# Kernel tuning notes

Measured on AMD Instinct MI355X. Metric: run time of the kernel, lower is better.

## Reference

```python
import jax, jax.numpy as jnp
import numpy as np

SHAPES = [(96, 96), (48, 48), (24, 24), (12, 12)]
B, C, NH, NP, NL, LYR, DFF = 4, 256, 8, 3, 4, 3, 1024
HD = C // NH
N = sum(h * w for h, w in SHAPES)


def setup_inputs():
    ks = iter(jax.random.split(jax.random.key(0), 64))
    p = lambda shape, s=0.02: jax.random.normal(next(ks), shape, jnp.float32) * s
    d = {}
    for i, (h, w) in enumerate(SHAPES):
        d[f'src{i}'] = jax.random.normal(next(ks), (B, C, h, w), jnp.float32)
        d[f'mask{i}'] = jnp.zeros((B, h, w), jnp.bool_)
        d[f'pos{i}'] = jax.random.normal(next(ks), (B, C, h, w), jnp.float32) * 0.02
    d['level_embed'] = p((NL, C), 1.0)  # torch init: normal_(std=1)
    d['W_off'] = p((LYR, C, NH * NL * NP * 2), 0.05); d['b_off'] = p((LYR, NH * NL * NP * 2), 0.05)
    d['W_attw'] = p((LYR, C, NH * NL * NP)); d['b_attw'] = jnp.zeros((LYR, NH * NL * NP))
    d['W_val'] = p((LYR, C, C)); d['b_val'] = jnp.zeros((LYR, C))
    d['W_out'] = p((LYR, C, C)); d['b_out'] = jnp.zeros((LYR, C))
    d['ln1_g'] = jnp.ones((LYR, C)); d['ln1_b'] = jnp.zeros((LYR, C))
    d['W_ff1'] = p((LYR, C, DFF)); d['b_ff1'] = jnp.zeros((LYR, DFF))
    d['W_ff2'] = p((LYR, DFF, C)); d['b_ff2'] = jnp.zeros((LYR, C))
    d['ln2_g'] = jnp.ones((LYR, C)); d['ln2_b'] = jnp.zeros((LYR, C))
    d['lnf_g'] = jnp.ones((C,)); d['lnf_b'] = jnp.zeros((C,))
    return d


def _layer_norm(x, g, b, eps=1e-5):
    m = jnp.mean(x, -1, keepdims=True)
    v = jnp.var(x, -1, keepdims=True)
    return (x - m) * jax.lax.rsqrt(v + eps) * g + b


def _ref_points():
    # centers of each cell per level, normalized to [0,1]; xy order -> [N,4] boxes with wh=0.1
    pts = []
    for h, w in SHAPES:
        ys = (jnp.arange(h, dtype=jnp.float32) + 0.5) / h
        xs = (jnp.arange(w, dtype=jnp.float32) + 0.5) / w
        yy, xx = jnp.meshgrid(ys, xs, indexing='ij')
        pts.append(jnp.stack([xx.ravel(), yy.ravel()], -1))
    r = jnp.concatenate(pts, 0)
    return jnp.concatenate([r, jnp.full_like(r, 0.1)], -1)


def _bilinear(value, H, W, loc):
    # value [B,H*W,NH,HD]; loc [B,Q,NH,NP,2] normalized; align_corners=False, zero padding
    x = loc[..., 0] * W - 0.5
    y = loc[..., 1] * H - 0.5
    x0f = jnp.floor(x); y0f = jnp.floor(y)
    wx = x - x0f; wy = y - y0f
    x0 = x0f.astype(jnp.int32); y0 = y0f.astype(jnp.int32)
    vt = jnp.transpose(value, (0, 2, 1, 3))  # [B,NH,HW,HD]
    Bq, Q = loc.shape[0], loc.shape[1]

    def g(yi, xi):
        valid = ((xi >= 0) & (xi < W) & (yi >= 0) & (yi < H)).astype(value.dtype)
        idx = jnp.clip(yi, 0, H - 1) * W + jnp.clip(xi, 0, W - 1)  # [B,Q,NH,NP]
        it = jnp.transpose(idx, (0, 2, 1, 3)).reshape(Bq, NH, Q * NP, 1)
        it = jnp.broadcast_to(it, (Bq, NH, Q * NP, HD))
        v = jnp.take_along_axis(vt, it, axis=2).reshape(Bq, NH, Q, NP, HD)
        v = jnp.transpose(v, (0, 2, 1, 3, 4))  # [B,Q,NH,NP,HD]
        return v * valid[..., None]

    return (g(y0, x0) * ((1 - wy) * (1 - wx))[..., None]
            + g(y0, x0 + 1) * ((1 - wy) * wx)[..., None]
            + g(y0 + 1, x0) * (wy * (1 - wx))[..., None]
            + g(y0 + 1, x0 + 1) * (wy * wx)[..., None])


def _msda(q, x, mask, ref, l, W_off, b_off, W_attw, b_attw, W_val, b_val, W_out, b_out):
    Bq, Nq, _ = q.shape
    value = x @ W_val[l] + b_val[l]
    value = jnp.where(mask[..., None], 0.0, value).reshape(Bq, Nq, NH, HD)
    off = (q @ W_off[l] + b_off[l]).reshape(Bq, Nq, NH, NL, NP, 2)
    aw = jax.nn.softmax((q @ W_attw[l] + b_attw[l]).reshape(Bq, Nq, NH, NL * NP), -1)
    aw = aw.reshape(Bq, Nq, NH, NL, NP)
    ref_xy = ref[None, :, None, None, None, :2]
    ref_wh = ref[None, :, None, None, None, 2:]
    loc = ref_xy + off / NP * ref_wh * 0.5  # [B,N,NH,NL,NP,2]
    out = jnp.zeros((Bq, Nq, NH, HD), x.dtype)
    s0 = 0
    for li, (h, w) in enumerate(SHAPES):
        samp = _bilinear(value[:, s0:s0 + h * w], h, w, loc[:, :, :, li])
        out = out + jnp.einsum('bqhpd,bqhp->bqhd', samp, aw[:, :, :, li])
        s0 += h * w
    return out.reshape(Bq, Nq, C) @ W_out[l] + b_out[l]


def _forward(srcs, masks, poss, level_embed, W_off, b_off, W_attw, b_attw, W_val, b_val,
             W_out, b_out, ln1_g, ln1_b, W_ff1, b_ff1, W_ff2, b_ff2, ln2_g, ln2_b, lnf_g, lnf_b):
    x = jnp.concatenate([s.reshape(B, C, -1).transpose(0, 2, 1) for s in srcs], 1)  # [B,N,C]
    mf = jnp.concatenate([m.reshape(B, -1) for m in masks], 1)                      # [B,N]
    pf = jnp.concatenate([p_.reshape(B, C, -1).transpose(0, 2, 1) + level_embed[i]
                          for i, p_ in enumerate(poss)], 1)
    ref = _ref_points()
    for l in range(LYR):
        q = x + pf
        x2 = _msda(q, x, mf, ref, l, W_off, b_off, W_attw, b_attw, W_val, b_val, W_out, b_out)
        x = _layer_norm(x + x2, ln1_g[l], ln1_b[l])
        h = jax.nn.gelu(x @ W_ff1[l] + b_ff1[l], approximate=False)
        x = _layer_norm(x + h @ W_ff2[l] + b_ff2[l], ln2_g[l], ln2_b[l])
    return _layer_norm(x, lnf_g, lnf_b)


def reference(src0, src1, src2, src3, mask0, mask1, mask2, mask3, pos0, pos1, pos2, pos3,
              level_embed, W_off, b_off, W_attw, b_attw, W_val, b_val, W_out, b_out,
              ln1_g, ln1_b, W_ff1, b_ff1, W_ff2, b_ff2, ln2_g, ln2_b, lnf_g, lnf_b):
    return _forward([src0, src1, src2, src3], [mask0, mask1, mask2, mask3],
                    [pos0, pos1, pos2, pos3], level_embed, W_off, b_off, W_attw, b_attw,
                    W_val, b_val, W_out, b_out, ln1_g, ln1_b, W_ff1, b_ff1, W_ff2, b_ff2,
                    ln2_g, ln2_b, lnf_g, lnf_b)
```

## Files before the change

### kernel.cpp

```cpp
#include <hip/hip_runtime.h>

#define B_   4
#define C_   256
#define NH_  8
#define HD_  32
#define NP_  3
#define NL_  4
#define LYR_ 3
#define DFF_ 1024
#define N_   12240
#define M_   (B_*N_)
#define MP_  49152
#define LT_  729088

typedef __attribute__((ext_vector_type(8))) short short8;
typedef __attribute__((ext_vector_type(4))) float f32x4;

__device__ __forceinline__ unsigned short f2bf(float f) {
    union { float f; unsigned u; } v; v.f = f;
    unsigned r = (v.u + 0x7fffu + ((v.u >> 16) & 1u)) >> 16;
    return (unsigned short)r;
}
__device__ __forceinline__ float bf2f(unsigned short h) {
    union { unsigned u; float f; } v; v.u = ((unsigned)h) << 16;
    return v.f;
}

__global__ __launch_bounds__(256) void k_concat(
    const float* __restrict__ s0, const float* __restrict__ s1,
    const float* __restrict__ s2, const float* __restrict__ s3,
    const float* __restrict__ p0, const float* __restrict__ p1,
    const float* __restrict__ p2, const float* __restrict__ p3,
    const float* __restrict__ lev, float* __restrict__ x, float* __restrict__ pf)
{
    int idx = blockIdx.x * 256 + threadIdx.x;
    int c  = idx & (C_ - 1);
    int bn = idx >> 8;
    int n  = bn % N_;
    int b  = bn / N_;
    int li, s, HW; const float *sp, *pp;
    if (n < 9216)       { li = 0; s = n;         HW = 9216; sp = s0; pp = p0; }
    else if (n < 11520) { li = 1; s = n - 9216;  HW = 2304; sp = s1; pp = p1; }
    else if (n < 12096) { li = 2; s = n - 11520; HW = 576;  sp = s2; pp = p2; }
    else                { li = 3; s = n - 12096; HW = 144;  sp = s3; pp = p3; }
    size_t o = (size_t)(b * C_ + c) * HW + s;
    x[idx]  = sp[o];
    pf[idx] = pp[o] + lev[li * C_ + c];
}

__global__ __launch_bounds__(256) void k_mask(
    float* __restrict__ v,
    const unsigned char* __restrict__ m0, const unsigned char* __restrict__ m1,
    const unsigned char* __restrict__ m2, const unsigned char* __restrict__ m3)
{
    int row = blockIdx.x;
    int n = row % N_, b = row / N_;
    int s, HW; const unsigned char* mp;
    if (n < 9216)       { s = n;         HW = 9216; mp = m0; }
    else if (n < 11520) { s = n - 9216;  HW = 2304; mp = m1; }
    else if (n < 12096) { s = n - 11520; HW = 576;  mp = m2; }
    else                { s = n - 12096; HW = 144;  mp = m3; }
    if (mp[b * HW + s])
        v[(size_t)row * C_ + threadIdx.x] = 0.f;
}

__global__ __launch_bounds__(256) void k_split(
    const float* __restrict__ W, unsigned short* __restrict__ Th,
    unsigned short* __restrict__ Tl, int K, int N)
{
    int per = K * N;
    int idx = blockIdx.x * 256 + threadIdx.x;
    if (idx >= LYR_ * per) return;
    int l = idx / per, r = idx - l * per;
    int k = r / N, n = r - k * N;
    float v = W[idx];
    unsigned short h = f2bf(v);
    unsigned short lo = f2bf(v - bf2f(h));
    size_t o = (size_t)l * LT_ + (size_t)n * K + k;
    Th[o] = h; Tl[o] = lo;
}

__device__ __forceinline__ int swz(int row, int bcol) {
    return row * 128 + (bcol ^ ((row & 7) << 4));
}

template <int MODE, bool ADD2>
__global__ __launch_bounds__(256) void k_mgemm(
    const float* __restrict__ A, const float* __restrict__ A2,
    const unsigned short* __restrict__ Bh, const unsigned short* __restrict__ Bl,
    const float* __restrict__ bias, const float* __restrict__ bias2, int bsplit,
    float* __restrict__ Cm, int Ndim, int Kdim)
{
    __shared__ __align__(16) unsigned short Ahs[128 * 64];
    __shared__ __align__(16) unsigned short Als[128 * 64];
    __shared__ __align__(16) unsigned short Bhs[128 * 64];
    __shared__ __align__(16) unsigned short Bls[128 * 64];

    const int tid = threadIdx.x;
    const int bm = blockIdx.y * 128;
    const int bn = blockIdx.x * 128;
    const int w  = tid >> 6, lane = tid & 63;
    const int wr = w >> 1, wc = w & 1;
    const int lm = lane & 15, lg = lane >> 4;

    const int srow = tid >> 1;
    const int sbc  = (tid & 1) * 64;

    f32x4 acc[4][4] = {};

    for (int k0 = 0; k0 < Kdim; k0 += 64) {
        {
            const float* Ap  = A  + (size_t)(bm + srow) * Kdim + k0 + (sbc >> 1);
            const float* A2p = A2 + (size_t)(bm + srow) * Kdim + k0 + (sbc >> 1);
            #pragma unroll
            for (int q = 0; q < 4; ++q) {
                float4 v0 = *(const float4*)(Ap + q * 8);
                float4 v1 = *(const float4*)(Ap + q * 8 + 4);
                if (ADD2) {
                    float4 u0 = *(const float4*)(A2p + q * 8);
                    float4 u1 = *(const float4*)(A2p + q * 8 + 4);
                    v0.x += u0.x; v0.y += u0.y; v0.z += u0.z; v0.w += u0.w;
                    v1.x += u1.x; v1.y += u1.y; v1.z += u1.z; v1.w += u1.w;
                }
                float f[8] = {v0.x, v0.y, v0.z, v0.w, v1.x, v1.y, v1.z, v1.w};
                short8 hv, lv;
                #pragma unroll
                for (int j = 0; j < 8; ++j) {
                    unsigned short h = f2bf(f[j]);
                    hv[j] = (short)h;
                    lv[j] = (short)f2bf(f[j] - bf2f(h));
                }
                int o = swz(srow, sbc + q * 16) >> 1;
                *(short8*)&Ahs[o] = hv;
                *(short8*)&Als[o] = lv;
            }
        }
        {
            int ng = bn + srow;
            bool ok = ng < Ndim;
            const unsigned short* bhp = Bh + (size_t)ng * Kdim + k0 + (sbc >> 1);
            const unsigned short* blp = Bl + (size_t)ng * Kdim + k0 + (sbc >> 1);
            #pragma unroll
            for (int q = 0; q < 4; ++q) {
                short8 hv = {}, lv = {};
                if (ok) {
                    hv = *(const short8*)(bhp + q * 8);
                    lv = *(const short8*)(blp + q * 8);
                }
                int o = swz(srow, sbc + q * 16) >> 1;
                *(short8*)&Bhs[o] = hv;
                *(short8*)&Bls[o] = lv;
            }
        }
        __syncthreads();
        #pragma unroll
        for (int ks = 0; ks < 2; ++ks) {
            const int cb = ks * 64 + lg * 16;
            short8 ah[4], al[4], bh[4], bl[4];
            #pragma unroll
            for (int i = 0; i < 4; ++i) {
                int o = swz(wr * 64 + i * 16 + lm, cb) >> 1;
                ah[i] = *(const short8*)&Ahs[o];
                al[i] = *(const short8*)&Als[o];
            }
            #pragma unroll
            for (int j = 0; j < 4; ++j) {
                int o = swz(wc * 64 + j * 16 + lm, cb) >> 1;
                bh[j] = *(const short8*)&Bhs[o];
                bl[j] = *(const short8*)&Bls[o];
            }
            #pragma unroll
            for (int i = 0; i < 4; ++i)
                #pragma unroll
                for (int j = 0; j < 4; ++j) {
                    acc[i][j] = __builtin_amdgcn_mfma_f32_16x16x32_bf16(al[i], bh[j], acc[i][j], 0, 0, 0);
                    acc[i][j] = __builtin_amdgcn_mfma_f32_16x16x32_bf16(ah[i], bl[j], acc[i][j], 0, 0, 0);
                    acc[i][j] = __builtin_amdgcn_mfma_f32_16x16x32_bf16(ah[i], bh[j], acc[i][j], 0, 0, 0);
                }
        }
        __syncthreads();
    }

    #pragma unroll
    for (int j = 0; j < 4; ++j) {
        int col = bn + wc * 64 + j * 16 + lm;
        if (col < Ndim) {
            float bb = (col < bsplit) ? bias[col] : bias2[col - bsplit];
            #pragma unroll
            for (int i = 0; i < 4; ++i) {
                #pragma unroll
                for (int p = 0; p < 4; ++p) {
                    int row = bm + wr * 64 + i * 16 + lg * 4 + p;
                    float v = acc[i][j][p] + bb;
                    if (MODE == 1)
                        v = 0.5f * v * (1.f + erff(v * 0.70710678118654752f));
                    Cm[(size_t)row * Ndim + col] = v;
                }
            }
        }
    }
}

__global__ __launch_bounds__(256) void k_sample(
    const float* __restrict__ value, const float* __restrict__ comb,
    float* __restrict__ out)
{
    int t = blockIdx.x * 256 + threadIdx.x;
    int gid = t >> 3, q4 = t & 3 * 2 + (t & 7);
    gid = t >> 3; q4 = t & 7;
    int h  = gid & 7;
    int bn = gid >> 3;
    int n  = bn % N_;
    int b  = bn / N_;

    int sr, Wr;
    if (n < 9216)       { sr = n;         Wr = 96; }
    else if (n < 11520) { sr = n - 9216;  Wr = 48; }
    else if (n < 12096) { sr = n - 11520; Wr = 24; }
    else                { sr = n - 12096; Wr = 12; }
    int iy = sr / Wr, ix = sr % Wr;
    float refx = (ix + 0.5f) / Wr;
    float refy = (iy + 0.5f) / Wr;

    const float* rowp = comb + (size_t)bn * 288;
    const float* offp = rowp + h * 24;
    const float* lgp  = rowp + 192 + h * 12;

    float lv[12];
    float mx = lgp[0];
    lv[0] = mx;
    #pragma unroll
    for (int i = 1; i < 12; ++i) { lv[i] = lgp[i]; mx = fmaxf(mx, lv[i]); }
    float ssum = 0.f;
    #pragma unroll
    for (int i = 0; i < 12; ++i) { lv[i] = __expf(lv[i] - mx); ssum += lv[i]; }
    float sinv = 1.f / ssum;

    const float* vbase = value + ((size_t)b * N_) * C_ + h * HD_ + q4 * 4;

    float4 acc = make_float4(0.f, 0.f, 0.f, 0.f);
    int s0 = 0;
    #pragma unroll
    for (int li = 0; li < 4; ++li) {
        const int Wl = 96 >> li;
        #pragma unroll
        for (int p = 0; p < NP_; ++p) {
            float ox = offp[(li * NP_ + p) * 2 + 0];
            float oy = offp[(li * NP_ + p) * 2 + 1];
            float xf = (refx + ox * (1.f / 60.f)) * Wl - 0.5f;
            float yf = (refy + oy * (1.f / 60.f)) * Wl - 0.5f;
            float x0f = floorf(xf), y0f = floorf(yf);
            float wx = xf - x0f, wy = yf - y0f;
            int x0 = (int)x0f, y0 = (int)y0f;
            float a = lv[li * NP_ + p] * sinv;
            #pragma unroll
            for (int dy = 0; dy < 2; ++dy) {
                #pragma unroll
                for (int dx = 0; dx < 2; ++dx) {
                    int yi = y0 + dy, xi = x0 + dx;
                    if (xi >= 0 && xi < Wl && yi >= 0 && yi < Wl) {
                        float wgt = a * (dy ? wy : 1.f - wy) * (dx ? wx : 1.f - wx);
                        float4 v = *(const float4*)(vbase + (size_t)(s0 + yi * Wl + xi) * C_);
                        acc.x += wgt * v.x; acc.y += wgt * v.y;
                        acc.z += wgt * v.z; acc.w += wgt * v.w;
                    }
                }
            }
        }
        s0 += Wl * Wl;
    }
    *(float4*)(out + (size_t)gid * HD_ + q4 * 4) = acc;
}

__global__ __launch_bounds__(256) void k_add_ln(
    const float* __restrict__ xin, const float* __restrict__ r,
    const float* __restrict__ g, const float* __restrict__ bta,
    float* __restrict__ out)
{
    int row = blockIdx.x;
    int c = threadIdx.x;
    size_t o = (size_t)row * C_ + c;
    float v = xin[o] + (r ? r[o] : 0.f);
    float s1 = v, s2 = v * v;
    #pragma unroll
    for (int ofs = 32; ofs > 0; ofs >>= 1) {
        s1 += __shfl_down(s1, ofs);
        s2 += __shfl_down(s2, ofs);
    }
    __shared__ float r1[4], r2[4];
    int wid = threadIdx.x >> 6, lane = threadIdx.x & 63;
    if (lane == 0) { r1[wid] = s1; r2[wid] = s2; }
    __syncthreads();
    float m   = (r1[0] + r1[1] + r1[2] + r1[3]) * (1.f / C_);
    float var = (r2[0] + r2[1] + r2[2] + r2[3]) * (1.f / C_) - m * m;
    float inv = rsqrtf(var + 1e-5f);
    out[o] = (v - m) * inv * g[c] + bta[c];
}

extern "C" void kernel_launch(void* const* d_in, const int* in_sizes, int n_in,
                              void* d_out, int out_size, void* d_ws, size_t ws_size,
                              hipStream_t stream)
{
    const float* src0 = (const float*)d_in[0];
    const unsigned char* mask0 = (const unsigned char*)d_in[1];
    const float* pos0 = (const float*)d_in[2];
    const float* src1 = (const float*)d_in[3];
    const unsigned char* mask1 = (const unsigned char*)d_in[4];
    const float* pos1 = (const float*)d_in[5];
    const float* src2 = (const float*)d_in[6];
    const unsigned char* mask2 = (const unsigned char*)d_in[7];
    const float* pos2 = (const float*)d_in[8];
    const float* src3 = (const float*)d_in[9];
    const unsigned char* mask3 = (const unsigned char*)d_in[10];
    const float* pos3 = (const float*)d_in[11];
    const float* lev    = (const float*)d_in[12];
    const float* W_off  = (const float*)d_in[13];
    const float* b_off  = (const float*)d_in[14];
    const float* W_attw = (const float*)d_in[15];
    const float* b_attw = (const float*)d_in[16];
    const float* W_val  = (const float*)d_in[17];
    const float* b_val  = (const float*)d_in[18];
    const float* W_out  = (const float*)d_in[19];
    const float* b_out  = (const float*)d_in[20];
    const float* ln1_g  = (const float*)d_in[21];
    const float* ln1_b  = (const float*)d_in[22];
    const float* W_ff1  = (const float*)d_in[23];
    const float* b_ff1  = (const float*)d_in[24];
    const float* W_ff2  = (const float*)d_in[25];
    const float* b_ff2  = (const float*)d_in[26];
    const float* ln2_g  = (const float*)d_in[27];
    const float* ln2_b  = (const float*)d_in[28];
    const float* lnf_g  = (const float*)d_in[29];
    const float* lnf_b  = (const float*)d_in[30];

    float* ws = (float*)d_ws;
    auto at = [&](size_t u) { return ws + u * (size_t)MP_; };
    float* x    = at(0);
    float* pf   = at(256);
    float* val  = at(512);
    float* msda = at(768);
    float* comb = at(1024);
    float* tmp  = at(1024);
    float* hbuf = at(512);

    unsigned short* Wh = (unsigned short*)(ws + (size_t)1312 * MP_);
    unsigned short* Wl = Wh + (size_t)LYR_ * LT_;
    const size_t OF_VAL = 0, OF_CMB = 65536, OF_ATT = 114688,
                 OF_OUT = 139264, OF_F1 = 204800, OF_F2 = 466944;

    const dim3 T(256);
    const int BIG = 1 << 30;

    k_split<<<(LYR_*65536 + 255)/256, T, 0, stream>>>(W_val,  Wh + OF_VAL, Wl + OF_VAL, 256, 256);
    k_split<<<(LYR_*49152 + 255)/256, T, 0, stream>>>(W_off,  Wh + OF_CMB, Wl + OF_CMB, 256, 192);
    k_split<<<(LYR_*24576 + 255)/256, T, 0, stream>>>(W_attw, Wh + OF_ATT, Wl + OF_ATT, 256, 96);
    k_split<<<(LYR_*65536 + 255)/256, T, 0, stream>>>(W_out,  Wh + OF_OUT, Wl + OF_OUT, 256, 256);
    k_split<<<(LYR_*262144 + 255)/256, T, 0, stream>>>(W_ff1, Wh + OF_F1,  Wl + OF_F1,  256, 1024);
    k_split<<<(LYR_*262144 + 255)/256, T, 0, stream>>>(W_ff2, Wh + OF_F2,  Wl + OF_F2,  1024, 256);

    k_concat<<<(M_*C_)/256, T, 0, stream>>>(src0, src1, src2, src3,
                                            pos0, pos1, pos2, pos3, lev, x, pf);

    for (int l = 0; l < LYR_; ++l) {
        const size_t lw = (size_t)l * LT_;

        k_mgemm<0, false><<<dim3(2, MP_/128), T, 0, stream>>>(
            x, x, Wh + lw + OF_VAL, Wl + lw + OF_VAL,
            b_val + l*C_, b_val + l*C_, BIG, val, 256, 256);
        k_mask<<<M_, T, 0, stream>>>(val, mask0, mask1, mask2, mask3);

        k_mgemm<0, true><<<dim3(3, MP_/128), T, 0, stream>>>(
            x, pf, Wh + lw + OF_CMB, Wl + lw + OF_CMB,
            b_off + l*192, b_attw + l*96, 192, comb, 288, 256);

        k_sample<<<(M_*NH_*8)/256, T, 0, stream>>>(val, comb, msda);

        k_mgemm<0, false><<<dim3(2, MP_/128), T, 0, stream>>>(
            msda, msda, Wh + lw + OF_OUT, Wl + lw + OF_OUT,
            b_out + l*C_, b_out + l*C_, BIG, tmp, 256, 256);

        k_add_ln<<<M_, T, 0, stream>>>(x, tmp, ln1_g + l*C_, ln1_b + l*C_, x);

        for (int ch = 0; ch < 3; ++ch) {
            const size_t row0 = (size_t)ch * 16384;
            k_mgemm<1, false><<<dim3(8, 128), T, 0, stream>>>(
                x + row0*C_, x + row0*C_, Wh + lw + OF_F1, Wl + lw + OF_F1,
                b_ff1 + l*DFF_, b_ff1 + l*DFF_, BIG, hbuf, 1024, 256);
            k_mgemm<0, false><<<dim3(2, 128), T, 0, stream>>>(
                hbuf, hbuf, Wh + lw + OF_F2, Wl + lw + OF_F2,
                b_ff2 + l*C_, b_ff2 + l*C_, BIG, tmp + row0*C_, 256, 1024);
        }

        k_add_ln<<<M_, T, 0, stream>>>(x, tmp, ln2_g + l*C_, ln2_b + l*C_, x);
    }

    k_add_ln<<<M_, T, 0, stream>>>(x, nullptr, lnf_g, lnf_b, (float*)d_out);
}
```

Measured before the change: 2.546 ms.

## Store GEMM A-operands as pre-split bf16 hi/lo pairs and tile-transpose concat

Activations that feed the split-bf16 GEMMs (x, msda output, FFN hidden) are now written by their producers (concat, layernorm, sampler, FF1 epilogue) directly as bf16 high/low pairs. The GEMM A-load no longer reads fp32 and converts it every k-tile, and the per-block conversion work repeated across column tiles is removed. The concat kernel also becomes a shared-memory tiled transpose so both the NCHW reads and the token-major writes are coalesced. In exchange, the residual stream x is held as hi+lo bf16, which is slightly less precise than fp32, and the q=x+pf path must rebuild the value and split it again.

```diff
diff --git a/kernel.cpp b/kernel.cpp
--- a/kernel.cpp
+++ b/kernel.cpp
@@ -26,26 +26,58 @@
     return v.f;
 }
 
-__global__ __launch_bounds__(256) void k_concat(
+__global__ __launch_bounds__(256) void k_concat_t(
     const float* __restrict__ s0, const float* __restrict__ s1,
     const float* __restrict__ s2, const float* __restrict__ s3,
     const float* __restrict__ p0, const float* __restrict__ p1,
     const float* __restrict__ p2, const float* __restrict__ p3,
-    const float* __restrict__ lev, float* __restrict__ x, float* __restrict__ pf)
-{
-    int idx = blockIdx.x * 256 + threadIdx.x;
-    int c  = idx & (C_ - 1);
-    int bn = idx >> 8;
-    int n  = bn % N_;
-    int b  = bn / N_;
-    int li, s, HW; const float *sp, *pp;
-    if (n < 9216)       { li = 0; s = n;         HW = 9216; sp = s0; pp = p0; }
-    else if (n < 11520) { li = 1; s = n - 9216;  HW = 2304; sp = s1; pp = p1; }
-    else if (n < 12096) { li = 2; s = n - 11520; HW = 576;  sp = s2; pp = p2; }
-    else                { li = 3; s = n - 12096; HW = 144;  sp = s3; pp = p3; }
-    size_t o = (size_t)(b * C_ + c) * HW + s;
-    x[idx]  = sp[o];
-    pf[idx] = pp[o] + lev[li * C_ + c];
+    const float* __restrict__ lev,
+    unsigned short* __restrict__ xh, unsigned short* __restrict__ xl,
+    float* __restrict__ pf)
+{
+    const int z = blockIdx.z;
+    const int b = z >> 2, li = z & 3;
+    const int HWs[4]  = {9216, 2304, 576, 144};
+    const int offs[4] = {0, 9216, 11520, 12096};
+    const int HW = HWs[li];
+    const int s0i = blockIdx.x * 32;
+    if (s0i >= HW) return;
+    const int ct = blockIdx.y * 32;
+    const float* sp = (li == 0) ? s0 : (li == 1) ? s1 : (li == 2) ? s2 : s3;
+    const float* pp = (li == 0) ? p0 : (li == 1) ? p1 : (li == 2) ? p2 : p3;
+
+    __shared__ float tsx[32][33], tsp[32][33];
+    const int tid = threadIdx.x;
+    const int tc  = tid & 31;
+    const int tr0 = tid >> 5;
+
+    #pragma unroll
+    for (int r = 0; r < 4; ++r) {
+        int cl = tr0 + r * 8;
+        int s  = s0i + tc;
+        float vx = 0.f, vp = 0.f;
+        if (s < HW) {
+            size_t o = (size_t)(b * C_ + ct + cl) * HW + s;
+            vx = sp[o]; vp = pp[o];
+        }
+        tsx[cl][tc] = vx; tsp[cl][tc] = vp;
+    }
+    __syncthreads();
+    const float lv = lev[li * C_ + ct + tc];
+    #pragma unroll
+    for (int r = 0; r < 4; ++r) {
+        int sl = tr0 + r * 8;
+        int s  = s0i + sl;
+        if (s < HW) {
+            int row = b * N_ + offs[li] + s;
+            size_t o = (size_t)row * C_ + ct + tc;
+            float vx = tsx[tc][sl];
+            unsigned short h = f2bf(vx);
+            xh[o] = h;
+            xl[o] = f2bf(vx - bf2f(h));
+            pf[o] = tsp[tc][sl] + lv;
+        }
+    }
 }
 
 __global__ __launch_bounds__(256) void k_mask(
@@ -84,12 +116,14 @@
     return row * 128 + (bcol ^ ((row & 7) << 4));
 }
 
-template <int MODE, bool ADD2>
+template <int MODE, int AKIND>
 __global__ __launch_bounds__(256) void k_mgemm(
-    const float* __restrict__ A, const float* __restrict__ A2,
+    const unsigned short* __restrict__ Ah, const unsigned short* __restrict__ Al,
+    const float* __restrict__ A2f,
     const unsigned short* __restrict__ Bh, const unsigned short* __restrict__ Bl,
     const float* __restrict__ bias, const float* __restrict__ bias2, int bsplit,
-    float* __restrict__ Cm, int Ndim, int Kdim)
+    float* __restrict__ Cf, unsigned short* __restrict__ Ch,
+    unsigned short* __restrict__ Cl, int Ndim, int Kdim)
 {
     __shared__ __align__(16) unsigned short Ahs[128 * 64];
     __shared__ __align__(16) unsigned short Als[128 * 64];
@@ -110,29 +144,38 @@
 
     for (int k0 = 0; k0 < Kdim; k0 += 64) {
         {
-            const float* Ap  = A  + (size_t)(bm + srow) * Kdim + k0 + (sbc >> 1);
-            const float* A2p = A2 + (size_t)(bm + srow) * Kdim + k0 + (sbc >> 1);
-            #pragma unroll
-            for (int q = 0; q < 4; ++q) {
-                float4 v0 = *(const float4*)(Ap + q * 8);
-                float4 v1 = *(const float4*)(Ap + q * 8 + 4);
-                if (ADD2) {
-                    float4 u0 = *(const float4*)(A2p + q * 8);
-                    float4 u1 = *(const float4*)(A2p + q * 8 + 4);
-                    v0.x += u0.x; v0.y += u0.y; v0.z += u0.z; v0.w += u0.w;
-                    v1.x += u1.x; v1.y += u1.y; v1.z += u1.z; v1.w += u1.w;
-                }
-                float f[8] = {v0.x, v0.y, v0.z, v0.w, v1.x, v1.y, v1.z, v1.w};
-                short8 hv, lv;
+            const unsigned short* ahp = Ah + (size_t)(bm + srow) * Kdim + k0 + (sbc >> 1);
+            const unsigned short* alp = Al + (size_t)(bm + srow) * Kdim + k0 + (sbc >> 1);
+            if (AKIND == 0) {
                 #pragma unroll
-                for (int j = 0; j < 8; ++j) {
-                    unsigned short h = f2bf(f[j]);
-                    hv[j] = (short)h;
-                    lv[j] = (short)f2bf(f[j] - bf2f(h));
-                }
-                int o = swz(srow, sbc + q * 16) >> 1;
-                *(short8*)&Ahs[o] = hv;
-                *(short8*)&Als[o] = lv;
+                for (int q = 0; q < 4; ++q) {
+                    short8 hv = *(const short8*)(ahp + q * 8);
+                    short8 lv = *(const short8*)(alp + q * 8);
+                    int o = swz(srow, sbc + q * 16) >> 1;
+                    *(short8*)&Ahs[o] = hv;
+                    *(short8*)&Als[o] = lv;
+                }
+            } else {
+                const float* a2p = A2f + (size_t)(bm + srow) * Kdim + k0 + (sbc >> 1);
+                #pragma unroll
+                for (int q = 0; q < 4; ++q) {
+                    short8 h8 = *(const short8*)(ahp + q * 8);
+                    short8 l8 = *(const short8*)(alp + q * 8);
+                    float4 u0 = *(const float4*)(a2p + q * 8);
+                    float4 u1 = *(const float4*)(a2p + q * 8 + 4);
+                    float f[8] = {u0.x, u0.y, u0.z, u0.w, u1.x, u1.y, u1.z, u1.w};
+                    short8 hv, lv;
+                    #pragma unroll
+                    for (int j = 0; j < 8; ++j) {
+                        float v = f[j] + bf2f((unsigned short)h8[j]) + bf2f((unsigned short)l8[j]);
+                        unsigned short h = f2bf(v);
+                        hv[j] = (short)h;
+                        lv[j] = (short)f2bf(v - bf2f(h));
+                    }
+                    int o = swz(srow, sbc + q * 16) >> 1;
+                    *(short8*)&Ahs[o] = hv;
+                    *(short8*)&Als[o] = lv;
+                }
             }
         }
         {
@@ -192,9 +235,14 @@
                 for (int p = 0; p < 4; ++p) {
                     int row = bm + wr * 64 + i * 16 + lg * 4 + p;
                     float v = acc[i][j][p] + bb;
-                    if (MODE == 1)
+                    if (MODE == 1) {
                         v = 0.5f * v * (1.f + erff(v * 0.70710678118654752f));
-                    Cm[(size_t)row * Ndim + col] = v;
+                        unsigned short h = f2bf(v);
+                        Ch[(size_t)row * Ndim + col] = h;
+                        Cl[(size_t)row * Ndim + col] = f2bf(v - bf2f(h));
+                    } else {
+                        Cf[(size_t)row * Ndim + col] = v;
+                    }
                 }
             }
         }
@@ -203,11 +251,11 @@
 
 __global__ __launch_bounds__(256) void k_sample(
     const float* __restrict__ value, const float* __restrict__ comb,
-    float* __restrict__ out)
+    unsigned short* __restrict__ msh, unsigned short* __restrict__ msl)
 {
     int t = blockIdx.x * 256 + threadIdx.x;
-    int gid = t >> 3, q4 = t & 3 * 2 + (t & 7);
-    gid = t >> 3; q4 = t & 7;
+    int gid = t >> 3;
+    int q4  = t & 7;
     int h  = gid & 7;
     int bn = gid >> 3;
     int n  = bn % N_;
@@ -269,18 +317,32 @@
         }
         s0 += Wl * Wl;
     }
-    *(float4*)(out + (size_t)gid * HD_ + q4 * 4) = acc;
-}
-
+    size_t ob = (size_t)gid * HD_ + q4 * 4;
+    float a4[4] = {acc.x, acc.y, acc.z, acc.w};
+    ushort4 hv, lv4;
+    unsigned short* hp = (unsigned short*)&hv;
+    unsigned short* lp = (unsigned short*)&lv4;
+    #pragma unroll
+    for (int j = 0; j < 4; ++j) {
+        unsigned short hh = f2bf(a4[j]);
+        hp[j] = hh;
+        lp[j] = f2bf(a4[j] - bf2f(hh));
+    }
+    *(ushort4*)&msh[ob] = hv;
+    *(ushort4*)&msl[ob] = lv4;
+}
+
+template <bool FINAL>
 __global__ __launch_bounds__(256) void k_add_ln(
-    const float* __restrict__ xin, const float* __restrict__ r,
+    unsigned short* __restrict__ xh, unsigned short* __restrict__ xl,
+    const float* __restrict__ r,
     const float* __restrict__ g, const float* __restrict__ bta,
-    float* __restrict__ out)
+    float* __restrict__ outf)
 {
     int row = blockIdx.x;
     int c = threadIdx.x;
     size_t o = (size_t)row * C_ + c;
-    float v = xin[o] + (r ? r[o] : 0.f);
+    float v = bf2f(xh[o]) + bf2f(xl[o]) + (r ? r[o] : 0.f);
     float s1 = v, s2 = v * v;
     #pragma unroll
     for (int ofs = 32; ofs > 0; ofs >>= 1) {
@@ -294,7 +356,14 @@
     float m   = (r1[0] + r1[1] + r1[2] + r1[3]) * (1.f / C_);
     float var = (r2[0] + r2[1] + r2[2] + r2[3]) * (1.f / C_) - m * m;
     float inv = rsqrtf(var + 1e-5f);
-    out[o] = (v - m) * inv * g[c] + bta[c];
+    float y = (v - m) * inv * g[c] + bta[c];
+    if (FINAL) {
+        outf[o] = y;
+    } else {
+        unsigned short h = f2bf(y);
+        xh[o] = h;
+        xl[o] = f2bf(y - bf2f(h));
+    }
 }
 
 extern "C" void kernel_launch(void* const* d_in, const int* in_sizes, int n_in,
@@ -335,13 +404,16 @@
 
     float* ws = (float*)d_ws;
     auto at = [&](size_t u) { return ws + u * (size_t)MP_; };
-    float* x    = at(0);
+    unsigned short* xh  = (unsigned short*)at(0);
+    unsigned short* xl  = (unsigned short*)at(128);
     float* pf   = at(256);
     float* val  = at(512);
-    float* msda = at(768);
+    unsigned short* msh = (unsigned short*)at(768);
+    unsigned short* msl = (unsigned short*)at(896);
     float* comb = at(1024);
     float* tmp  = at(1024);
-    float* hbuf = at(512);
+    unsigned short* hbh = (unsigned short*)at(512);
+    unsigned short* hbl = hbh + (size_t)16384 * DFF_;
 
     unsigned short* Wh = (unsigned short*)(ws + (size_t)1312 * MP_);
     unsigned short* Wl = Wh + (size_t)LYR_ * LT_;
@@ -358,41 +430,41 @@
     k_split<<<(LYR_*262144 + 255)/256, T, 0, stream>>>(W_ff1, Wh + OF_F1,  Wl + OF_F1,  256, 1024);
     k_split<<<(LYR_*262144 + 255)/256, T, 0, stream>>>(W_ff2, Wh + OF_F2,  Wl + OF_F2,  1024, 256);
 
-    k_concat<<<(M_*C_)/256, T, 0, stream>>>(src0, src1, src2, src3,
-                                            pos0, pos1, pos2, pos3, lev, x, pf);
+    k_concat_t<<<dim3(288, 8, 16), T, 0, stream>>>(
+        src0, src1, src2, src3, pos0, pos1, pos2, pos3, lev, xh, xl, pf);
 
     for (int l = 0; l < LYR_; ++l) {
         const size_t lw = (size_t)l * LT_;
 
-        k_mgemm<0, false><<<dim3(2, MP_/128), T, 0, stream>>>(
-            x, x, Wh + lw + OF_VAL, Wl + lw + OF_VAL,
-            b_val + l*C_, b_val + l*C_, BIG, val, 256, 256);
+        k_mgemm<0, 0><<<dim3(2, MP_/128), T, 0, stream>>>(
+            xh, xl, nullptr, Wh + lw + OF_VAL, Wl + lw + OF_VAL,
+            b_val + l*C_, b_val + l*C_, BIG, val, nullptr, nullptr, 256, 256);
         k_mask<<<M_, T, 0, stream>>>(val, mask0, mask1, mask2, mask3);
 
-        k_mgemm<0, true><<<dim3(3, MP_/128), T, 0, stream>>>(
-            x, pf, Wh + lw + OF_CMB, Wl + lw + OF_CMB,
-            b_off + l*192, b_attw + l*96, 192, comb, 288, 256);
-
-        k_sample<<<(M_*NH_*8)/256, T, 0, stream>>>(val, comb, msda);
-
-        k_mgemm<0, false><<<dim3(2, MP_/128), T, 0, stream>>>(
-            msda, msda, Wh + lw + OF_OUT, Wl + lw + OF_OUT,
-            b_out + l*C_, b_out + l*C_, BIG, tmp, 256, 256);
-
-        k_add_ln<<<M_, T, 0, stream>>>(x, tmp, ln1_g + l*C_, ln1_b + l*C_, x);
+        k_mgemm<0, 1><<<dim3(3, MP_/128), T, 0, stream>>>(
+            xh, xl, pf, Wh + lw + OF_CMB, Wl + lw + OF_CMB,
+            b_off + l*192, b_attw + l*96, 192, comb, nullptr, nullptr, 288, 256);
+
+        k_sample<<<(M_*NH_*8)/256, T, 0, stream>>>(val, comb, msh, msl);
+
+        k_mgemm<0, 0><<<dim3(2, MP_/128), T, 0, stream>>>(
+            msh, msl, nullptr, Wh + lw + OF_OUT, Wl + lw + OF_OUT,
+            b_out + l*C_, b_out + l*C_, BIG, tmp, nullptr, nullptr, 256, 256);
+
+        k_add_ln<false><<<M_, T, 0, stream>>>(xh, xl, tmp, ln1_g + l*C_, ln1_b + l*C_, nullptr);
 
         for (int ch = 0; ch < 3; ++ch) {
             const size_t row0 = (size_t)ch * 16384;
-            k_mgemm<1, false><<<dim3(8, 128), T, 0, stream>>>(
-                x + row0*C_, x + row0*C_, Wh + lw + OF_F1, Wl + lw + OF_F1,
-                b_ff1 + l*DFF_, b_ff1 + l*DFF_, BIG, hbuf, 1024, 256);
-            k_mgemm<0, false><<<dim3(2, 128), T, 0, stream>>>(
-                hbuf, hbuf, Wh + lw + OF_F2, Wl + lw + OF_F2,
-                b_ff2 + l*C_, b_ff2 + l*C_, BIG, tmp + row0*C_, 256, 1024);
-        }
-
-        k_add_ln<<<M_, T, 0, stream>>>(x, tmp, ln2_g + l*C_, ln2_b + l*C_, x);
-    }
-
-    k_add_ln<<<M_, T, 0, stream>>>(x, nullptr, lnf_g, lnf_b, (float*)d_out);
-}
+            k_mgemm<1, 0><<<dim3(8, 128), T, 0, stream>>>(
+                xh + row0*C_, xl + row0*C_, nullptr, Wh + lw + OF_F1, Wl + lw + OF_F1,
+                b_ff1 + l*DFF_, b_ff1 + l*DFF_, BIG, nullptr, hbh, hbl, 1024, 256);
+            k_mgemm<0, 0><<<dim3(2, 128), T, 0, stream>>>(
+                hbh, hbl, nullptr, Wh + lw + OF_F2, Wl + lw + OF_F2,
+                b_ff2 + l*C_, b_ff2 + l*C_, BIG, tmp + row0*C_, nullptr, nullptr, 256, 1024);
+        }
+
+        k_add_ln<false><<<M_, T, 0, stream>>>(xh, xl, tmp, ln2_g + l*C_, ln2_b + l*C_, nullptr);
+    }
+
+    k_add_ln<true><<<M_, T, 0, stream>>>(xh, xl, nullptr, lnf_g, lnf_b, (float*)d_out);
+}
```

Result: faster. 2.402 ms (-5.7%).
